# Kernel optimization log

Measured on AMD Instinct MI355X. Metric: run time of the kernel, lower is better.

## Reference

```python
import jax, jax.numpy as jnp
import numpy as np

N_EMBD = 1024
N_HEAD = 16
HEAD_DIM = N_EMBD // N_HEAD


def setup_inputs() -> dict:
    key = jax.random.key(0)
    k1, k2, k3 = jax.random.split(key, 3)
    x = jax.random.normal(k1, (2, 2048, N_EMBD), dtype=jnp.float32)
    # torch nn.Linear(in, out) weight has shape (out, in); y = x @ W.T
    w_qkv = jax.random.normal(k2, (3 * N_EMBD, N_EMBD), dtype=jnp.float32) * (1.0 / np.sqrt(N_EMBD))
    w_proj = jax.random.normal(k3, (N_EMBD, N_EMBD), dtype=jnp.float32) * (1.0 / np.sqrt(N_EMBD))
    return {"x": x, "w_qkv": w_qkv, "w_proj": w_proj}


def reference(x, w_qkv, w_proj):
    B, T, C = x.shape
    qkv = jnp.einsum('btc,dc->btd', x, w_qkv)  # [B,T,3C]
    q, k, v = jnp.split(qkv, 3, axis=2)
    # [B,H,T,hd]
    q = q.reshape(B, T, N_HEAD, HEAD_DIM).transpose(0, 2, 1, 3)
    k = k.reshape(B, T, N_HEAD, HEAD_DIM).transpose(0, 2, 1, 3)
    v = v.reshape(B, T, N_HEAD, HEAD_DIM).transpose(0, 2, 1, 3)
    att = jnp.einsum('bhqd,bhkd->bhqk', q, k) / jnp.sqrt(jnp.float32(HEAD_DIM))
    causal = jnp.tril(jnp.ones((T, T), dtype=bool))  # [T,T]
    att = jnp.where(causal[None, None], att, -jnp.inf)
    att = jax.nn.softmax(att, axis=-1)
    y = jnp.einsum('bhqk,bhkd->bhqd', att, v)
    y = y.transpose(0, 2, 1, 3).reshape(B, T, C)
    return jnp.einsum('btc,dc->btd', y, w_proj)
```

## Files before the change

### kernel.cpp

```cpp
#include <hip/hip_runtime.h>
#include <stdint.h>


typedef unsigned short u16;
typedef __bf16 bf16_t;
typedef bf16_t bf16x8 __attribute__((ext_vector_type(8)));
typedef float f32x4 __attribute__((ext_vector_type(4)));
typedef float f32x16 __attribute__((ext_vector_type(16)));

__device__ __forceinline__ u16 f2bf(float f) {
  return __builtin_bit_cast(u16, (bf16_t)f);
}

__device__ __forceinline__ float hexp2(float x) {
  float r;
  asm("v_exp_f32 %0, %1" : "=v"(r) : "v"(x));
  return r;
}
__device__ __forceinline__ uint32_t cvtpk(float lo, float hi) {
  uint32_t d;
  asm("v_cvt_pk_bf16_f32 %0, %1, %2" : "=v"(d) : "v"(lo), "v"(hi));
  return d;
}
__device__ __forceinline__ void plswap(uint32_t& a, uint32_t& b) {
  asm("v_permlane32_swap_b32 %0, %1" : "+v"(a), "+v"(b));
}

template<int CC>
__device__ __forceinline__ bf16x8 mkPfrag(const float* p) {
  uint32_t A1 = cvtpk(p[8 * CC + 0], p[8 * CC + 1]);
  uint32_t A2 = cvtpk(p[8 * CC + 2], p[8 * CC + 3]);
  uint32_t B1 = cvtpk(p[8 * CC + 4], p[8 * CC + 5]);
  uint32_t B2 = cvtpk(p[8 * CC + 6], p[8 * CC + 7]);
  plswap(A1, B1);
  plswap(A2, B2);
  union { uint32_t u[4]; bf16x8 v; } r;
  r.u[0] = A1; r.u[1] = A2; r.u[2] = B1; r.u[3] = B2;
  return r.v;
}

__device__ __forceinline__ void gload_lds16(const void* g, void* l) {
  __builtin_amdgcn_global_load_lds(
      (const __attribute__((address_space(1))) uint32_t*)(uint64_t)g,
      (__attribute__((address_space(3))) uint32_t*)(uint32_t)(uint64_t)l,
      16, 0, 0);
}

__global__ void cast_all(const float* __restrict__ x, const float* __restrict__ wq,
                         const float* __restrict__ wp, u16* __restrict__ xb,
                         u16* __restrict__ wqb, u16* __restrict__ wpb) {
  int i = blockIdx.x * blockDim.x + threadIdx.x;
  const float* s; u16* d; int off;
  if (i < 1048576)            { s = x;  d = xb;  off = i; }
  else if (i < 1048576 + 786432) { s = wq; d = wqb; off = i - 1048576; }
  else                        { s = wp; d = wpb; off = i - (1048576 + 786432); }
  float4 f = reinterpret_cast<const float4*>(s)[off];
  ushort4 o;
  o.x = f2bf(f.x); o.y = f2bf(f.y); o.z = f2bf(f.z); o.w = f2bf(f.w);
  reinterpret_cast<ushort4*>(d)[off] = o;
}

template<int MODE>
__global__ void gemm_bt(const u16* __restrict__ A, const u16* __restrict__ Bm,
                        u16* __restrict__ qb, u16* __restrict__ kb, u16* __restrict__ vb,
                        float* __restrict__ outf) {
  __shared__ __attribute__((aligned(16))) u16 As[128 * 64];
  __shared__ __attribute__((aligned(16))) u16 Bs[128 * 64];
  const int tid = threadIdx.x;
  const int lane = tid & 63;
  const int w = tid >> 6;
  const int wr = w >> 1, wc = w & 1;
  const int g = lane >> 4, r = lane & 15;
  const int tn = blockIdx.x, tm = blockIdx.y;

  f32x4 acc[4][4] = {};

  const char* Ab = (const char*)(A + (size_t)tm * 128 * 1024);
  const char* Bb = (const char*)(Bm + (size_t)tn * 128 * 1024);
  char* AsB = (char*)As;
  char* BsB = (char*)Bs;

  for (int k0 = 0; k0 < 1024; k0 += 64) {
#pragma unroll
    for (int i = 0; i < 4; ++i) {
      const int L = (i * 256 + tid) * 16;
      const int row = L >> 7;
      const int colb = (L & 127) ^ ((row & 7) << 4);
      gload_lds16(Ab + (size_t)row * 2048 + k0 * 2 + colb, AsB + L);
      gload_lds16(Bb + (size_t)row * 2048 + k0 * 2 + colb, BsB + L);
    }
    __syncthreads();
#pragma unroll
    for (int kk = 0; kk < 2; ++kk) {
      bf16x8 a[4], b[4];
#pragma unroll
      for (int m = 0; m < 4; ++m) {
        const int rowA = wr * 64 + m * 16 + r;
        const int kbyt = (kk * 64 + g * 16) ^ ((rowA & 7) << 4);
        a[m] = *(const bf16x8*)(AsB + rowA * 128 + kbyt);
      }
#pragma unroll
      for (int n = 0; n < 4; ++n) {
        const int rowB = wc * 64 + n * 16 + r;
        const int kbyt = (kk * 64 + g * 16) ^ ((rowB & 7) << 4);
        b[n] = *(const bf16x8*)(BsB + rowB * 128 + kbyt);
      }
      __builtin_amdgcn_s_setprio(1);
#pragma unroll
      for (int m = 0; m < 4; ++m)
#pragma unroll
        for (int n = 0; n < 4; ++n)
          acc[m][n] = __builtin_amdgcn_mfma_f32_16x16x32_bf16(a[m], b[n], acc[m][n], 0, 0, 0);
      __builtin_amdgcn_s_setprio(0);
    }
    __syncthreads();
  }

  const int mrow0 = tm * 128 + wr * 64;
  const int ncol0 = tn * 128 + wc * 64;

  if (MODE == 1) {
#pragma unroll
    for (int m = 0; m < 4; ++m)
#pragma unroll
      for (int n = 0; n < 4; ++n) {
        const int nc = ncol0 + n * 16 + r;
#pragma unroll
        for (int j = 0; j < 4; ++j) {
          const int mr = mrow0 + m * 16 + g * 4 + j;
          outf[(size_t)mr * 1024 + nc] = acc[m][n][j];
        }
      }
  } else {
    const int sel = (blockIdx.x * 128) >> 10;
    const float qscl = (sel == 0) ? 0.18033688f : 1.0f;
    if (sel < 2) {
      u16* dst = (sel == 0) ? qb : kb;
#pragma unroll
      for (int m = 0; m < 4; ++m)
#pragma unroll
        for (int n = 0; n < 4; ++n) {
          const int nc = (ncol0 + n * 16 + r) & 1023;
          const int h = nc >> 6, d = nc & 63;
#pragma unroll
          for (int j = 0; j < 4; ++j) {
            const int mr = mrow0 + m * 16 + g * 4 + j;
            const int bb = mr >> 11, t = mr & 2047;
            dst[((size_t)(bb * 16 + h) * 2048 + t) * 64 + d] = f2bf(acc[m][n][j] * qscl);
          }
        }
    } else {
#pragma unroll
      for (int m = 0; m < 4; ++m)
#pragma unroll
        for (int n = 0; n < 4; ++n) {
          const int nc = (ncol0 + n * 16 + r) & 1023;
          const int h = nc >> 6, d = nc & 63;
#pragma unroll
          for (int j = 0; j < 4; ++j) {
            const int mr = mrow0 + m * 16 + g * 4 + j;
            const int bb = mr >> 11, t = mr & 2047;
            vb[((size_t)(bb * 16 + h) * 64 + d) * 2048 + t] = f2bf(acc[m][n][j]);
          }
        }
    }
  }
}

__global__ __launch_bounds__(256, 2)
void attn_fwd(const u16* __restrict__ qb, const u16* __restrict__ kb,
              const u16* __restrict__ vb, u16* __restrict__ yb) {
  __shared__ __attribute__((aligned(16))) u16 Ks[64 * 64];
  __shared__ __attribute__((aligned(16))) u16 Vs[64 * 64];
  __shared__ __attribute__((aligned(16))) float Linv[4][32];
  const int tid = threadIdx.x;
  const int lane = tid & 63;
  const int w = tid >> 6;
  const int hi = lane >> 5;
  const int q5 = lane & 31;
  const int hi4 = hi * 4;
  const int bh = blockIdx.x;
  const int bb = bh >> 4, h = bh & 15;
  const int y = blockIdx.y;
  const int base = (y + bh) & 15;
  const int a = (bh & 16) ? (15 - base) : base;
  const int qb0 = a * 128;
  const int qw = qb0 + w * 32;
  const int qg = qw + q5;

  const char* Kb = (const char*)(kb + (size_t)bh * (2048 * 64));
  const char* Vb = (const char*)(vb + (size_t)bh * (64 * 2048));
  const u16* Q = qb + (size_t)bh * (2048 * 64);
  char* KsB = (char*)Ks;
  char* VsB = (char*)Vs;

  bf16x8 qf[4];
#pragma unroll
  for (int f = 0; f < 4; ++f)
    qf[f] = *(const bf16x8*)(&Q[(size_t)qg * 64 + f * 16 + hi * 8]);

  f32x16 o0 = {}, o1 = {};
  float psum = 0.0f;

  const int nt = (qw >> 6) + 1;
  const int ntmax = (qb0 >> 6) + 2;
  const int swz = (q5 & 7) << 4;

  for (int t = 0; t < ntmax; ++t) {
    const int k0 = t * 64;
#pragma unroll
    for (int i = 0; i < 2; ++i) {
      const int L = (i * 256 + tid) * 16;
      const int row = L >> 7;
      const int colb = (L & 127) ^ ((row & 7) << 4);
      gload_lds16(Kb + (size_t)(k0 + row) * 128 + colb, KsB + L);
      gload_lds16(Vb + (size_t)row * 4096 + (size_t)k0 * 2 + colb, VsB + L);
    }
    __syncthreads();

    if (t < nt) {
      f32x16 s0 = {}, s1 = {};
      __builtin_amdgcn_s_setprio(1);
#pragma unroll
      for (int f = 0; f < 4; ++f) {
        const int cb = f * 32 + hi * 16;
        bf16x8 ka0 = *(const bf16x8*)(KsB + q5 * 128 + (cb ^ swz));
        bf16x8 ka1 = *(const bf16x8*)(KsB + (32 + q5) * 128 + (cb ^ swz));
        s0 = __builtin_amdgcn_mfma_f32_32x32x16_bf16(ka0, qf[f], s0, 0, 0, 0);
        s1 = __builtin_amdgcn_mfma_f32_32x32x16_bf16(ka1, qf[f], s1, 0, 0, 0);
      }
      __builtin_amdgcn_s_setprio(0);

      float p0[16], p1[16];
      if (t == nt - 1) {
#pragma unroll
        for (int i = 0; i < 16; ++i) {
          const int kl = (i & 3) + 8 * (i >> 2) + hi4;
          float e0 = hexp2(s0[i]);
          float e1 = hexp2(s1[i]);
          p0[i] = (k0 + kl <= qg) ? e0 : 0.0f;
          p1[i] = (k0 + 32 + kl <= qg) ? e1 : 0.0f;
          psum += p0[i] + p1[i];
        }
      } else {
#pragma unroll
        for (int i = 0; i < 16; ++i) {
          p0[i] = hexp2(s0[i]);
          p1[i] = hexp2(s1[i]);
          psum += p0[i] + p1[i];
        }
      }

      bf16x8 pf0 = mkPfrag<0>(p0);
      bf16x8 pf1 = mkPfrag<1>(p0);
      bf16x8 pf2 = mkPfrag<0>(p1);
      bf16x8 pf3 = mkPfrag<1>(p1);

      __builtin_amdgcn_s_setprio(1);
#pragma unroll
      for (int c = 0; c < 4; ++c) {
        const int cb = c * 32 + hi * 16;
        bf16x8 v0f = *(const bf16x8*)(VsB + q5 * 128 + (cb ^ swz));
        bf16x8 v1f = *(const bf16x8*)(VsB + (32 + q5) * 128 + (cb ^ swz));
        const bf16x8 pf = (c == 0) ? pf0 : (c == 1) ? pf1 : (c == 2) ? pf2 : pf3;
        o0 = __builtin_amdgcn_mfma_f32_32x32x16_bf16(pf, v0f, o0, 0, 0, 0);
        o1 = __builtin_amdgcn_mfma_f32_32x32x16_bf16(pf, v1f, o1, 0, 0, 0);
      }
      __builtin_amdgcn_s_setprio(0);
    }
    __syncthreads();
  }

  const float tot = psum + __shfl_xor(psum, 32);
  if (lane < 32) Linv[w][q5] = 1.0f / tot;
  asm volatile("s_waitcnt lgkmcnt(0)" ::: "memory");
  __builtin_amdgcn_sched_barrier(0);
  f32x4 lv[4];
#pragma unroll
  for (int r2 = 0; r2 < 4; ++r2)
    lv[r2] = *(const f32x4*)(&Linv[w][r2 * 8 + hi4]);

#pragma unroll
  for (int reg = 0; reg < 16; ++reg) {
    const int r4 = reg & 3, r2 = reg >> 2;
    const float li = lv[r2][r4];
    const int trow = qw + r4 + 8 * r2 + hi4;
    const size_t bpos = ((size_t)(bb * 2048 + trow)) * 1024 + h * 64 + q5;
    yb[bpos]      = f2bf(o0[reg] * li);
    yb[bpos + 32] = f2bf(o1[reg] * li);
  }
}

extern "C" void kernel_launch(void* const* d_in, const int* in_sizes, int n_in,
                              void* d_out, int out_size, void* d_ws, size_t ws_size,
                              hipStream_t stream) {
  const float* x     = (const float*)d_in[0];
  const float* wqkv  = (const float*)d_in[1];
  const float* wproj = (const float*)d_in[2];
  float* out = (float*)d_out;
  char* ws = (char*)d_ws;
  u16* xb     = (u16*)(ws + (size_t)(0u  << 20));
  u16* wqkvb  = (u16*)(ws + (size_t)(8u  << 20));
  u16* wprojb = (u16*)(ws + (size_t)(14u << 20));
  u16* qb     = (u16*)(ws + (size_t)(16u << 20));
  u16* kb     = (u16*)(ws + (size_t)(24u << 20));
  u16* vb     = (u16*)(ws + (size_t)(32u << 20));
  u16* yb     = (u16*)(ws + (size_t)(40u << 20));

  cast_all<<<8192, 256, 0, stream>>>(x, wqkv, wproj, xb, wqkvb, wprojb);

  gemm_bt<0><<<dim3(24, 32), 256, 0, stream>>>(xb, wqkvb, qb, kb, vb, nullptr);
  attn_fwd<<<dim3(32, 16), 256, 0, stream>>>(qb, kb, vb, yb);
  gemm_bt<1><<<dim3(8, 32), 256, 0, stream>>>(yb, wprojb, nullptr, nullptr, nullptr, out);
}
```

Before: 104.4 us.

## Double-buffer attention K/V loads, coalesce V-transpose stores via LDS, rebalance causal tiles

The attention kernel now double-buffers K/V tiles in LDS, prefetching the next tile while the current one is computed and waiting on vmcnt instead of a full barrier drain. The QKV GEMM epilogue for V stages the transposed tile through swizzled shared memory, so global stores become coalesced 16-byte writes instead of scattered 2-byte writes. The mapping of query blocks to workgroups is changed to pair short and long causal rows for better load balance. Doubling the attention LDS footprint may lower occupancy, and the final iteration issues a redundant prefetch of tile 0.

```diff
diff --git a/kernel.cpp b/kernel.cpp
--- a/kernel.cpp
+++ b/kernel.cpp
@@ -64,8 +64,7 @@
 __global__ void gemm_bt(const u16* __restrict__ A, const u16* __restrict__ Bm,
                         u16* __restrict__ qb, u16* __restrict__ kb, u16* __restrict__ vb,
                         float* __restrict__ outf) {
-  __shared__ __attribute__((aligned(16))) u16 As[128 * 64];
-  __shared__ __attribute__((aligned(16))) u16 Bs[128 * 64];
+  __shared__ __attribute__((aligned(16))) u16 SMEM[2 * 128 * 64];
   const int tid = threadIdx.x;
   const int lane = tid & 63;
   const int w = tid >> 6;
@@ -77,8 +76,8 @@
 
   const char* Ab = (const char*)(A + (size_t)tm * 128 * 1024);
   const char* Bb = (const char*)(Bm + (size_t)tn * 128 * 1024);
-  char* AsB = (char*)As;
-  char* BsB = (char*)Bs;
+  char* AsB = (char*)SMEM;
+  char* BsB = AsB + 16384;
 
   for (int k0 = 0; k0 < 1024; k0 += 64) {
 #pragma unroll
@@ -150,19 +149,31 @@
           }
         }
     } else {
+      u16* Wv = SMEM + w * 4096;
 #pragma unroll
       for (int m = 0; m < 4; ++m)
 #pragma unroll
         for (int n = 0; n < 4; ++n) {
-          const int nc = (ncol0 + n * 16 + r) & 1023;
-          const int h = nc >> 6, d = nc & 63;
-#pragma unroll
-          for (int j = 0; j < 4; ++j) {
-            const int mr = mrow0 + m * 16 + g * 4 + j;
-            const int bb = mr >> 11, t = mr & 2047;
-            vb[((size_t)(bb * 16 + h) * 64 + d) * 2048 + t] = f2bf(acc[m][n][j]);
-          }
+          const int dl = n * 16 + r;
+          uint32_t lo = cvtpk(acc[m][n][0], acc[m][n][1]);
+          uint32_t hi2 = cvtpk(acc[m][n][2], acc[m][n][3]);
+          char* p = (char*)Wv + dl * 128 + ((m * 32 + g * 8) ^ ((dl & 7) << 4));
+          *(uint32_t*)p = lo;
+          *(uint32_t*)(p + 4) = hi2;
         }
+      asm volatile("s_waitcnt lgkmcnt(0)" ::: "memory");
+      __builtin_amdgcn_sched_barrier(0);
+      const int hh = (ncol0 - 2048) >> 6;
+      const int t0 = mrow0 & 2047;
+      const int bb2 = mrow0 >> 11;
+      u16* vdst = vb + ((size_t)(bb2 * 16 + hh) * 64) * 2048 + t0;
+#pragma unroll
+      for (int rd = 0; rd < 8; ++rd) {
+        const int dl = rd * 8 + (lane >> 3);
+        const int tb = lane & 7;
+        const char* src = (char*)Wv + dl * 128 + ((tb ^ (dl & 7)) << 4);
+        *(uint4*)(vdst + (size_t)dl * 2048 + tb * 8) = *(const uint4*)src;
+      }
     }
   }
 }
@@ -170,8 +181,7 @@
 __global__ __launch_bounds__(256, 2)
 void attn_fwd(const u16* __restrict__ qb, const u16* __restrict__ kb,
               const u16* __restrict__ vb, u16* __restrict__ yb) {
-  __shared__ __attribute__((aligned(16))) u16 Ks[64 * 64];
-  __shared__ __attribute__((aligned(16))) u16 Vs[64 * 64];
+  __shared__ __attribute__((aligned(16))) u16 KV[2][2][64 * 64];
   __shared__ __attribute__((aligned(16))) float Linv[4][32];
   const int tid = threadIdx.x;
   const int lane = tid & 63;
@@ -181,9 +191,8 @@
   const int hi4 = hi * 4;
   const int bh = blockIdx.x;
   const int bb = bh >> 4, h = bh & 15;
-  const int y = blockIdx.y;
-  const int base = (y + bh) & 15;
-  const int a = (bh & 16) ? (15 - base) : base;
+  const int base = (blockIdx.y + bh) & 15;
+  const int a = (base < 8) ? 2 * base : 31 - 2 * base;
   const int qb0 = a * 128;
   const int qw = qb0 + w * 32;
   const int qg = qw + q5;
@@ -191,8 +200,6 @@
   const char* Kb = (const char*)(kb + (size_t)bh * (2048 * 64));
   const char* Vb = (const char*)(vb + (size_t)bh * (64 * 2048));
   const u16* Q = qb + (size_t)bh * (2048 * 64);
-  char* KsB = (char*)Ks;
-  char* VsB = (char*)Vs;
 
   bf16x8 qf[4];
 #pragma unroll
@@ -206,69 +213,81 @@
   const int ntmax = (qb0 >> 6) + 2;
   const int swz = (q5 & 7) << 4;
 
-  for (int t = 0; t < ntmax; ++t) {
-    const int k0 = t * 64;
+  auto stage = [&](int k0, int buf) {
 #pragma unroll
     for (int i = 0; i < 2; ++i) {
       const int L = (i * 256 + tid) * 16;
       const int row = L >> 7;
       const int colb = (L & 127) ^ ((row & 7) << 4);
-      gload_lds16(Kb + (size_t)(k0 + row) * 128 + colb, KsB + L);
-      gload_lds16(Vb + (size_t)row * 4096 + (size_t)k0 * 2 + colb, VsB + L);
-    }
-    __syncthreads();
-
-    if (t < nt) {
-      f32x16 s0 = {}, s1 = {};
-      __builtin_amdgcn_s_setprio(1);
-#pragma unroll
-      for (int f = 0; f < 4; ++f) {
-        const int cb = f * 32 + hi * 16;
-        bf16x8 ka0 = *(const bf16x8*)(KsB + q5 * 128 + (cb ^ swz));
-        bf16x8 ka1 = *(const bf16x8*)(KsB + (32 + q5) * 128 + (cb ^ swz));
-        s0 = __builtin_amdgcn_mfma_f32_32x32x16_bf16(ka0, qf[f], s0, 0, 0, 0);
-        s1 = __builtin_amdgcn_mfma_f32_32x32x16_bf16(ka1, qf[f], s1, 0, 0, 0);
-      }
-      __builtin_amdgcn_s_setprio(0);
-
-      float p0[16], p1[16];
-      if (t == nt - 1) {
-#pragma unroll
-        for (int i = 0; i < 16; ++i) {
-          const int kl = (i & 3) + 8 * (i >> 2) + hi4;
-          float e0 = hexp2(s0[i]);
-          float e1 = hexp2(s1[i]);
-          p0[i] = (k0 + kl <= qg) ? e0 : 0.0f;
-          p1[i] = (k0 + 32 + kl <= qg) ? e1 : 0.0f;
-          psum += p0[i] + p1[i];
-        }
-      } else {
-#pragma unroll
-        for (int i = 0; i < 16; ++i) {
-          p0[i] = hexp2(s0[i]);
-          p1[i] = hexp2(s1[i]);
-          psum += p0[i] + p1[i];
-        }
-      }
-
-      bf16x8 pf0 = mkPfrag<0>(p0);
-      bf16x8 pf1 = mkPfrag<1>(p0);
-      bf16x8 pf2 = mkPfrag<0>(p1);
-      bf16x8 pf3 = mkPfrag<1>(p1);
-
-      __builtin_amdgcn_s_setprio(1);
-#pragma unroll
-      for (int c = 0; c < 4; ++c) {
-        const int cb = c * 32 + hi * 16;
-        bf16x8 v0f = *(const bf16x8*)(VsB + q5 * 128 + (cb ^ swz));
-        bf16x8 v1f = *(const bf16x8*)(VsB + (32 + q5) * 128 + (cb ^ swz));
-        const bf16x8 pf = (c == 0) ? pf0 : (c == 1) ? pf1 : (c == 2) ? pf2 : pf3;
-        o0 = __builtin_amdgcn_mfma_f32_32x32x16_bf16(pf, v0f, o0, 0, 0, 0);
-        o1 = __builtin_amdgcn_mfma_f32_32x32x16_bf16(pf, v1f, o1, 0, 0, 0);
-      }
-      __builtin_amdgcn_s_setprio(0);
-    }
-    __syncthreads();
+      gload_lds16(Kb + (size_t)(k0 + row) * 128 + colb, (char*)KV[buf][0] + L);
+      gload_lds16(Vb + (size_t)row * 4096 + (size_t)k0 * 2 + colb,
+                  (char*)KV[buf][1] + L);
+    }
+  };
+
+  auto compute = [&](int t, int k0, const char* KsB, const char* VsB) {
+    f32x16 s0 = {}, s1 = {};
+    __builtin_amdgcn_s_setprio(1);
+#pragma unroll
+    for (int f = 0; f < 4; ++f) {
+      const int cb = f * 32 + hi * 16;
+      bf16x8 ka0 = *(const bf16x8*)(KsB + q5 * 128 + (cb ^ swz));
+      bf16x8 ka1 = *(const bf16x8*)(KsB + (32 + q5) * 128 + (cb ^ swz));
+      s0 = __builtin_amdgcn_mfma_f32_32x32x16_bf16(ka0, qf[f], s0, 0, 0, 0);
+      s1 = __builtin_amdgcn_mfma_f32_32x32x16_bf16(ka1, qf[f], s1, 0, 0, 0);
+    }
+    __builtin_amdgcn_s_setprio(0);
+
+    float p0[16], p1[16];
+    if (t == nt - 1) {
+#pragma unroll
+      for (int i = 0; i < 16; ++i) {
+        const int kl = (i & 3) + 8 * (i >> 2) + hi4;
+        float e0 = hexp2(s0[i]);
+        float e1 = hexp2(s1[i]);
+        p0[i] = (k0 + kl <= qg) ? e0 : 0.0f;
+        p1[i] = (k0 + 32 + kl <= qg) ? e1 : 0.0f;
+        psum += p0[i] + p1[i];
+      }
+    } else {
+#pragma unroll
+      for (int i = 0; i < 16; ++i) {
+        p0[i] = hexp2(s0[i]);
+        p1[i] = hexp2(s1[i]);
+        psum += p0[i] + p1[i];
+      }
+    }
+
+    bf16x8 pf0 = mkPfrag<0>(p0);
+    bf16x8 pf1 = mkPfrag<1>(p0);
+    bf16x8 pf2 = mkPfrag<0>(p1);
+    bf16x8 pf3 = mkPfrag<1>(p1);
+
+    __builtin_amdgcn_s_setprio(1);
+#pragma unroll
+    for (int c = 0; c < 4; ++c) {
+      const int cb = c * 32 + hi * 16;
+      bf16x8 v0f = *(const bf16x8*)(VsB + q5 * 128 + (cb ^ swz));
+      bf16x8 v1f = *(const bf16x8*)(VsB + (32 + q5) * 128 + (cb ^ swz));
+      const bf16x8 pf = (c == 0) ? pf0 : (c == 1) ? pf1 : (c == 2) ? pf2 : pf3;
+      o0 = __builtin_amdgcn_mfma_f32_32x32x16_bf16(pf, v0f, o0, 0, 0, 0);
+      o1 = __builtin_amdgcn_mfma_f32_32x32x16_bf16(pf, v1f, o1, 0, 0, 0);
+    }
+    __builtin_amdgcn_s_setprio(0);
+  };
+
+  stage(0, 0);
+  int t = 0;
+  while (true) {
+    const int k0n = (t + 1 < ntmax) ? (t + 1) * 64 : 0;
+    stage(k0n, (t + 1) & 1);
+    asm volatile("s_waitcnt vmcnt(4)" ::: "memory");
+    __builtin_amdgcn_s_barrier();
+    __builtin_amdgcn_sched_barrier(0);
+    if (t < nt) compute(t, t * 64, (const char*)KV[t & 1][0], (const char*)KV[t & 1][1]);
+    __builtin_amdgcn_sched_barrier(0);
+    __builtin_amdgcn_s_barrier();
+    if (++t >= ntmax) break;
   }
 
   const float tot = psum + __shfl_xor(psum, 32);
```

After: 95.72 us. -8.4%, faster.
